# Kernel tuning notes

Measured on AMD Instinct MI355X. Metric: run time of the kernel, lower is better.

## Reference

```python
import jax, jax.numpy as jnp
import numpy as np

H = 1024       # hidden_size
R = 4          # downsacale_ratio -> bottleneck H//R = 256
DI = 2048      # mamba d_inner = expand * H
NS = 16        # d_state
KC = 4         # d_conv
DTR = 64       # dt_rank = ceil(H/16)
B, L = 4, 1024


def setup_inputs() -> dict:
    key = jax.random.key(0)
    ks = iter(jax.random.split(key, 32))
    w = lambda shape, s=0.02: jax.random.normal(next(ks), shape, jnp.float32) * s
    Hr = H // R
    inp = {
        'x': jax.random.normal(next(ks), (B, L, H), jnp.float32),
        't': jax.random.normal(next(ks), (B, H), jnp.float32),
        # adaLN modulation: SiLU -> Linear(H, 3H)
        'ada_w': w((H, 3 * H)), 'ada_b': jnp.zeros((3 * H,), jnp.float32),
        # hg_dense: Linear(H,H/R) SiLU Linear(H/R,H)
        'hgd_w1': w((H, Hr)), 'hgd_b1': jnp.zeros((Hr,), jnp.float32),
        'hgd_w2': w((Hr, H)), 'hgd_b2': jnp.zeros((H,), jnp.float32),
        # Mamba params
        'in_proj_w': w((H, 2 * DI)),
        'conv_w': w((DI, KC), 0.1), 'conv_b': jnp.zeros((DI,), jnp.float32),
        'x_proj_w': w((DI, DTR + 2 * NS)),
        'dt_proj_w': w((DTR, DI), 0.1),
        'dt_proj_b': jnp.log(jnp.expm1(jnp.full((DI,), 0.01, jnp.float32))),  # softplus^-1(0.01)
        'A_log': jnp.log(jnp.broadcast_to(jnp.arange(1, NS + 1, dtype=jnp.float32), (DI, NS))),
        'Dp': jnp.ones((DI,), jnp.float32),
        'out_proj_w': w((DI, H)),
        # hg_fuse
        'fm_w': w((H, Hr)), 'fm_b': jnp.zeros((Hr,), jnp.float32),
        'fr_w': w((H, Hr)), 'fr_b': jnp.zeros((Hr,), jnp.float32),
        'ff_w': w((Hr, H)), 'ff_b': jnp.zeros((H,), jnp.float32),
    }
    return inp


def _ln(x, eps=1e-6):
    mu = jnp.mean(x, -1, keepdims=True)
    var = jnp.mean(jnp.square(x - mu), -1, keepdims=True)
    return (x - mu) / jnp.sqrt(var + eps)


def _mamba(xd, in_proj_w, conv_w, conv_b, x_proj_w, dt_proj_w, dt_proj_b, A_log, Dp, out_proj_w):
    # xd: [B, L, H]
    xz = xd @ in_proj_w                      # [B, L, 2*DI]
    xm, z = jnp.split(xz, 2, axis=-1)
    # causal depthwise conv over time
    xc = jnp.swapaxes(xm, 1, 2)              # [B, DI, L]
    xc = jax.lax.conv_general_dilated(
        xc, conv_w[:, None, :], window_strides=(1,), padding=[(KC - 1, 0)],
        feature_group_count=DI, dimension_numbers=('NCH', 'OIH', 'NCH'))
    xc = jax.nn.silu(jnp.swapaxes(xc, 1, 2) + conv_b)   # [B, L, DI]
    dbl = xc @ x_proj_w                      # [B, L, DTR + 2*NS]
    dt = jax.nn.softplus(dbl[..., :DTR] @ dt_proj_w + dt_proj_b)   # [B, L, DI]
    Bm = dbl[..., DTR:DTR + NS]              # [B, L, NS]
    Cm = dbl[..., DTR + NS:]                 # [B, L, NS]
    A = -jnp.exp(A_log)                      # [DI, NS]

    def step(h, inp):
        dt_t, x_t, B_t, C_t = inp            # [B,DI],[B,DI],[B,NS],[B,NS]
        dA = jnp.exp(dt_t[:, :, None] * A)                       # [B, DI, NS]
        h = dA * h + (dt_t * x_t)[:, :, None] * B_t[:, None, :]
        y = jnp.einsum('bdn,bn->bd', h, C_t)
        return h, y

    h0 = jnp.zeros((xd.shape[0], DI, NS), xd.dtype)
    seq = (jnp.moveaxis(dt, 1, 0), jnp.moveaxis(xc, 1, 0),
           jnp.moveaxis(Bm, 1, 0), jnp.moveaxis(Cm, 1, 0))
    _, ys = jax.lax.scan(step, h0, seq)
    y = jnp.moveaxis(ys, 0, 1) + xc * Dp     # [B, L, DI]
    y = y * jax.nn.silu(z)
    return y @ out_proj_w                    # [B, L, H]


def reference(x, t, ada_w, ada_b, hgd_w1, hgd_b1, hgd_w2, hgd_b2,
              in_proj_w, conv_w, conv_b, x_proj_w, dt_proj_w, dt_proj_b,
              A_log, Dp, out_proj_w, fm_w, fm_b, fr_w, fr_b, ff_w, ff_b):
    ada = jax.nn.silu(t) @ ada_w + ada_b               # [B, 3H]
    shift, scale, alpha = jnp.split(ada, 3, axis=-1)
    x1 = _ln(x) * (1 + scale[:, None, :]) + shift[:, None, :]
    xd = jax.nn.silu(x1 @ hgd_w1 + hgd_b1) @ hgd_w2 + hgd_b2
    x1_2 = _mamba(xd, in_proj_w, conv_w, conv_b, x_proj_w, dt_proj_w,
                  dt_proj_b, A_log, Dp, out_proj_w)
    a = jax.nn.silu(x1_2 @ fm_w + fm_b)
    b = jax.nn.silu(x1 @ fr_w + fr_b)
    fuse = (a * b) @ ff_w + ff_b
    return x + alpha[:, None, :] * fuse
```

## Files before the change

kernel.cpp:

```cpp
#include <hip/hip_runtime.h>
#include <math.h>
#include <stdint.h>

#define H_   1024
#define HR_  256
#define DI_  2048
#define NS_  16
#define KC_  4
#define DTR_ 64
#define B_   4
#define L_   1024
#define ROWS (B_*L_)
#define H3_  3072
#define NCH_ 32
#define CL_  32
#define CLT_ 8

typedef short bf16x8 __attribute__((ext_vector_type(8)));
typedef float f32x4  __attribute__((ext_vector_type(4)));

#if __has_builtin(__builtin_amdgcn_exp2f)
#define EXP2(x) __builtin_amdgcn_exp2f(x)
#else
#define EXP2(x) __expf((x) * 0.6931471805599453f)
#endif
#define LOG2E 1.4426950408889634f

__device__ __forceinline__ float silu_f(float v) { return v / (1.f + __expf(-v)); }

__device__ __forceinline__ uint32_t pack_bf16_2(float a, float b) {
    uint32_t ua = __float_as_uint(a);
    uint32_t ub = __float_as_uint(b);
    uint32_t ra = (ua + 0x7FFFu + ((ua >> 16) & 1u)) >> 16;
    uint32_t rb = (ub + 0x7FFFu + ((ub >> 16) & 1u)) >> 16;
    return ra | (rb << 16);
}
__device__ __forceinline__ unsigned short cvt_bf16(float a) {
    uint32_t ua = __float_as_uint(a);
    return (unsigned short)((ua + 0x7FFFu + ((ua >> 16) & 1u)) >> 16);
}
__device__ __forceinline__ float bf16_to_f(unsigned short u) {
    return __uint_as_float(((uint32_t)u) << 16);
}

__device__ __forceinline__ void gload16(const short* g, short* l) {
    __builtin_amdgcn_global_load_lds(
        (const __attribute__((address_space(1))) void*)g,
        (__attribute__((address_space(3))) void*)l, 16, 0, 0);
}

#define TW_HGDFR 0ull
#define TW_HGD2  524288ull
#define TW_INPJ  786432ull
#define TW_XPJ   4980736ull
#define TW_DTPJ  5242880ull
#define TW_OPJ   5373952ull
#define TW_FM    7471104ull
#define TW_FF    7733248ull
#define TWT      7995392ull

__global__ __launch_bounds__(256) void wtrans_kernel(
    const float* __restrict__ s0, const float* __restrict__ s1,
    const float* __restrict__ s2, const float* __restrict__ s3,
    const float* __restrict__ s4, const float* __restrict__ s5,
    const float* __restrict__ s6, const float* __restrict__ s7,
    const float* __restrict__ s8, short* __restrict__ wt)
{
    int bid = blockIdx.x;
    const float* src; short* dst; int K, N, rel;
    if      (bid < 256)  { src = s0; dst = wt + TW_HGDFR;          K = 1024; N = 256;  rel = bid; }
    else if (bid < 512)  { src = s1; dst = wt + TW_HGDFR + 262144; K = 1024; N = 256;  rel = bid - 256; }
    else if (bid < 768)  { src = s2; dst = wt + TW_HGD2;           K = 256;  N = 1024; rel = bid - 512; }
    else if (bid < 4864) { src = s3; dst = wt + TW_INPJ;           K = 1024; N = 4096; rel = bid - 768; }
    else if (bid < 5120) { src = s4; dst = wt + TW_XPJ;            K = 2048; N = 96;   rel = bid - 4864; }
    else if (bid < 5248) { src = s5; dst = wt + TW_DTPJ;           K = 64;   N = 2048; rel = bid - 5120; }
    else if (bid < 7296) { src = s6; dst = wt + TW_OPJ;            K = 2048; N = 1024; rel = bid - 5248; }
    else if (bid < 7552) { src = s7; dst = wt + TW_FM;             K = 1024; N = 256;  rel = bid - 7296; }
    else                 { src = s8; dst = wt + TW_FF;             K = 256;  N = 1024; rel = bid - 7552; }
    int tkc = K >> 5;
    int tk = rel % tkc, tn = rel / tkc;

    __shared__ float ld[32][33];
    int tx = threadIdx.x & 7, ty = threadIdx.x >> 3;
    int kk = tk * 32 + ty, nn = tn * 32 + tx * 4;
    float4 v = make_float4(0.f, 0.f, 0.f, 0.f);
    if (nn < N) v = *(const float4*)&src[(size_t)kk * N + nn];
    ld[ty][tx * 4 + 0] = v.x; ld[ty][tx * 4 + 1] = v.y;
    ld[ty][tx * 4 + 2] = v.z; ld[ty][tx * 4 + 3] = v.w;
    __syncthreads();
    int nn2 = tn * 32 + ty, kk2 = tk * 32 + tx * 4;
    float a0 = ld[tx * 4 + 0][ty], a1 = ld[tx * 4 + 1][ty];
    float a2 = ld[tx * 4 + 2][ty], a3 = ld[tx * 4 + 3][ty];
    uint2 p = { pack_bf16_2(a0, a1), pack_bf16_2(a2, a3) };
    *(uint2*)&dst[(size_t)nn2 * K + kk2] = p;
}

__global__ __launch_bounds__(256) void cwt_kernel(
    const float* __restrict__ conv_w, float* __restrict__ cwt)
{
    int d = blockIdx.x * 256 + threadIdx.x;
    float4 v = *(const float4*)&conv_w[d * KC_];
    cwt[0 * DI_ + d] = v.x;
    cwt[1 * DI_ + d] = v.y;
    cwt[2 * DI_ + d] = v.z;
    cwt[3 * DI_ + d] = v.w;
}

__global__ __launch_bounds__(256) void ada_part_kernel(
    const float* __restrict__ t, const float* __restrict__ ada_w,
    float* __restrict__ part)
{
    int col = blockIdx.x * 1024 + threadIdx.x * 4;
    int b = blockIdx.y, z = blockIdx.z;
    __shared__ float st[32];
    if (threadIdx.x < 32) {
        float v = t[b * H_ + z * 32 + threadIdx.x];
        st[threadIdx.x] = silu_f(v);
    }
    __syncthreads();
    float4 acc = make_float4(0.f, 0.f, 0.f, 0.f);
    const float* w = ada_w + (size_t)(z * 32) * H3_ + col;
    #pragma unroll
    for (int k = 0; k < 32; ++k) {
        float4 wv = *(const float4*)(w + (size_t)k * H3_);
        float s = st[k];
        acc.x = fmaf(s, wv.x, acc.x);
        acc.y = fmaf(s, wv.y, acc.y);
        acc.z = fmaf(s, wv.z, acc.z);
        acc.w = fmaf(s, wv.w, acc.w);
    }
    *(float4*)&part[((size_t)z * B_ + b) * H3_ + col] = acc;
}

__global__ __launch_bounds__(256) void ada_red_kernel(
    const float* __restrict__ part, const float* __restrict__ ada_b,
    float* __restrict__ ada)
{
    int i = (blockIdx.x * 256 + threadIdx.x) * 4;
    int b = i / H3_, col = i - b * H3_;
    float4 s = make_float4(0.f, 0.f, 0.f, 0.f);
    #pragma unroll
    for (int z = 0; z < 32; ++z) {
        float4 p = *(const float4*)&part[((size_t)z * B_ + b) * H3_ + col];
        s.x += p.x; s.y += p.y; s.z += p.z; s.w += p.w;
    }
    float4 bv = *(const float4*)&ada_b[col];
    s.x += bv.x; s.y += bv.y; s.z += bv.z; s.w += bv.w;
    *(float4*)&ada[(size_t)b * H3_ + col] = s;
}

__global__ __launch_bounds__(256) void ln_mod_kernel(
    const float* __restrict__ x, const float* __restrict__ ada,
    short* __restrict__ x1b)
{
    int row = blockIdx.x;
    int b   = row >> 10;
    const float* xr = x + (size_t)row * H_;
    float4 v = ((const float4*)xr)[threadIdx.x];
    float s  = v.x + v.y + v.z + v.w;
    float s2 = v.x*v.x + v.y*v.y + v.z*v.z + v.w*v.w;

    __shared__ float red[8];
    int wave = threadIdx.x >> 6, lane = threadIdx.x & 63;
    #pragma unroll
    for (int off = 32; off; off >>= 1) {
        s  += __shfl_down(s,  off);
        s2 += __shfl_down(s2, off);
    }
    if (lane == 0) { red[wave] = s; red[4 + wave] = s2; }
    __syncthreads();
    float ts  = red[0] + red[1] + red[2] + red[3];
    float ts2 = red[4] + red[5] + red[6] + red[7];
    float mu  = ts  * (1.f / H_);
    float var = ts2 * (1.f / H_) - mu * mu;
    float inv = rsqrtf(var + 1e-6f);

    const float* sh = ada + b * H3_;
    int i = threadIdx.x * 4;
    float4 sh4 = *(const float4*)&sh[i];
    float4 sc4 = *(const float4*)&sh[H_ + i];
    float ox = (v.x - mu) * inv * (1.f + sc4.x) + sh4.x;
    float oy = (v.y - mu) * inv * (1.f + sc4.y) + sh4.y;
    float oz = (v.z - mu) * inv * (1.f + sc4.z) + sh4.z;
    float ow = (v.w - mu) * inv * (1.f + sc4.w) + sh4.w;
    uint2 p = { pack_bf16_2(ox, oy), pack_bf16_2(oz, ow) };
    *(uint2*)(x1b + (size_t)row * H_ + i) = p;
}

template<int ACT, bool SPLITK>
__global__ __launch_bounds__(256) void gemm128(
    const short* __restrict__ A, int lda,
    const short* __restrict__ Wt, int ldw,
    const float* __restrict__ bias,
    float* __restrict__ C, short* __restrict__ Cb, short* __restrict__ Cb2,
    int ldc, int M, int N, int K,
    const float* __restrict__ E0, const float* __restrict__ E1)
{
    __shared__ short As[3][4096];
    __shared__ short Bs[3][4096];
    int tid  = threadIdx.x;
    int lane = tid & 63, wv = tid >> 6, wm = wv >> 1, wn = wv & 1;
    int n0 = blockIdx.x * 128;
    int m0 = blockIdx.y * 128;

    if (SPLITK) {
        int z = blockIdx.z;
        A  += (size_t)z * K;
        Wt += (size_t)z * K;
        C  += (size_t)z * M * N;
    }

    int r = lane & 15, g = lane >> 4;
    int sA = wv * 2;
    const short* ga0 = A  + (size_t)(m0 + sA * 16 + r) * lda + g * 8;
    const short* ga1 = ga0 + (size_t)16 * lda;
    const short* gb0 = Wt + (size_t)(n0 + sA * 16 + r) * ldw + g * 8;
    const short* gb1 = gb0 + (size_t)16 * ldw;

    f32x4 acc[4][4];
    #pragma unroll
    for (int i = 0; i < 4; ++i)
        #pragma unroll
        for (int j = 0; j < 4; ++j) {
            acc[i][j][0] = 0.f; acc[i][j][1] = 0.f;
            acc[i][j][2] = 0.f; acc[i][j][3] = 0.f;
        }

    #define STAGE(buf, koff)                                    \
        do {                                                    \
            gload16(ga0 + (koff), &As[buf][sA * 512]);          \
            gload16(ga1 + (koff), &As[buf][sA * 512 + 512]);    \
            gload16(gb0 + (koff), &Bs[buf][sA * 512]);          \
            gload16(gb1 + (koff), &Bs[buf][sA * 512 + 512]);    \
        } while (0)

    #define COMPUTE(buf)                                                          \
        do {                                                                      \
            bf16x8 af[4], bfr[4];                                                 \
            _Pragma("unroll")                                                     \
            for (int i = 0; i < 4; ++i)                                           \
                af[i] = *(const bf16x8*)&As[buf][(wm * 4 + i) * 512 + lane * 8];  \
            _Pragma("unroll")                                                     \
            for (int j = 0; j < 4; ++j)                                           \
                bfr[j] = *(const bf16x8*)&Bs[buf][(wn * 4 + j) * 512 + lane * 8]; \
            _Pragma("unroll")                                                     \
            for (int i = 0; i < 4; ++i)                                           \
                _Pragma("unroll")                                                 \
                for (int j = 0; j < 4; ++j)                                       \
                    acc[i][j] = __builtin_amdgcn_mfma_f32_16x16x32_bf16(          \
                        af[i], bfr[j], acc[i][j], 0, 0, 0);                       \
        } while (0)

    int T = K >> 5;
    STAGE(0, 0);
    if (T > 1) STAGE(1, 32);
    for (int t = 0; t < T; ++t) {
        if (t + 1 < T) asm volatile("s_waitcnt vmcnt(4)" ::: "memory");
        else           asm volatile("s_waitcnt vmcnt(0)" ::: "memory");
        __builtin_amdgcn_s_barrier();
        if (t + 2 < T) STAGE((t + 2) % 3, (t + 2) * 32);
        COMPUTE(t % 3);
    }
    #undef STAGE
    #undef COMPUTE

    #pragma unroll
    for (int i = 0; i < 4; ++i) {
        int mb = m0 + wm * 64 + i * 16 + ((lane >> 4) << 2);
        #pragma unroll
        for (int j = 0; j < 4; ++j) {
            int n = n0 + wn * 64 + j * 16 + (lane & 15);
            if (n < N) {
                float bv;
                if (ACT == 6) bv = (n < 256) ? bias[n] : E0[n - 256];
                else          bv = bias ? bias[n] : 0.f;
                #pragma unroll
                for (int rr = 0; rr < 4; ++rr) {
                    int m = mb + rr;
                    float v = acc[i][j][rr] + bv;
                    size_t ci = (size_t)m * ldc + n;
                    if (ACT == 6) {
                        float sv = silu_f(v);
                        if (n < 256) Cb[(size_t)m * 256 + n]        = (short)cvt_bf16(sv);
                        else         Cb2[(size_t)m * 256 + (n-256)] = (short)cvt_bf16(sv);
                    } else {
                        if (ACT == 2) v = (v > 20.f) ? v : log1pf(__expf(v));
                        else if (ACT == 4) {
                            int bb = m >> 10;
                            v = E0[ci] + E1[bb * H3_ + 2 * H_ + n] * v;
                        }
                        if (C)  C[ci]  = v;
                        if (Cb) Cb[ci] = (short)cvt_bf16(v);
                    }
                }
            }
        }
    }
}

template<int ACT, bool SPLITK>
__global__ __launch_bounds__(512) void gemm256d(
    const short* __restrict__ A, int lda,
    const short* __restrict__ Wt, int ldw,
    short* __restrict__ Cb, int ldc,
    int M, int N, int K)
{
    extern __shared__ short lds[];
    short* Asb = lds;
    short* Bsb = lds + 16384;
    int tid  = threadIdx.x;
    int lane = tid & 63, wv = tid >> 6;
    int wm = wv >> 2, wn = wv & 3;
    int n0 = blockIdx.x * 256;
    int m0 = blockIdx.y * 256;

    if (SPLITK) {
        int z = blockIdx.z;
        A  += (size_t)z * K;
        Wt += (size_t)z * K;
        Cb += (size_t)z * M * N;
    }

    int r = lane & 15, g = lane >> 4;
    int sA = wv * 2;
    const short* ga0 = A  + (size_t)(m0 + sA * 16 + r) * lda + g * 8;
    const short* ga1 = ga0 + (size_t)16 * lda;
    const short* gb0 = Wt + (size_t)(n0 + sA * 16 + r) * ldw + g * 8;
    const short* gb1 = gb0 + (size_t)16 * ldw;

    f32x4 acc[8][4];
    #pragma unroll
    for (int i = 0; i < 8; ++i)
        #pragma unroll
        for (int j = 0; j < 4; ++j) {
            acc[i][j][0] = 0.f; acc[i][j][1] = 0.f;
            acc[i][j][2] = 0.f; acc[i][j][3] = 0.f;
        }

    #define STAGE2(buf, koff)                                       \
        do {                                                        \
            gload16(ga0 + (koff), &Asb[(buf) * 8192 + sA * 512]);   \
            gload16(ga1 + (koff), &Asb[(buf) * 8192 + sA * 512 + 512]); \
            gload16(gb0 + (koff), &Bsb[(buf) * 8192 + sA * 512]);   \
            gload16(gb1 + (koff), &Bsb[(buf) * 8192 + sA * 512 + 512]); \
        } while (0)

    int T = K >> 5;
    STAGE2(0, 0);
    __syncthreads();
    int cur = 0;
    for (int t = 0; t < T; ++t) {
        if (t + 1 < T) STAGE2(cur ^ 1, (t + 1) * 32);
        {
            bf16x8 af[8], bfr[4];
            #pragma unroll
            for (int i = 0; i < 8; ++i)
                af[i] = *(const bf16x8*)&Asb[cur * 8192 + (wm * 8 + i) * 512 + lane * 8];
            #pragma unroll
            for (int j = 0; j < 4; ++j)
                bfr[j] = *(const bf16x8*)&Bsb[cur * 8192 + (wn * 4 + j) * 512 + lane * 8];
            __builtin_amdgcn_s_setprio(1);
            #pragma unroll
            for (int i = 0; i < 8; ++i)
                #pragma unroll
                for (int j = 0; j < 4; ++j)
                    acc[i][j] = __builtin_amdgcn_mfma_f32_16x16x32_bf16(
                        af[i], bfr[j], acc[i][j], 0, 0, 0);
            __builtin_amdgcn_s_setprio(0);
        }
        __syncthreads();
        cur ^= 1;
    }
    #undef STAGE2

    #pragma unroll
    for (int i = 0; i < 8; ++i) {
        int mb = m0 + wm * 128 + i * 16 + ((lane >> 4) << 2);
        #pragma unroll
        for (int j = 0; j < 4; ++j) {
            int n = n0 + wn * 64 + j * 16 + (lane & 15);
            #pragma unroll
            for (int rr = 0; rr < 4; ++rr) {
                int m = mb + rr;
                float v = acc[i][j][rr];
                if (ACT == 5) {
                    size_t idx = (n < DI_) ? ((size_t)m * DI_ + n)
                                           : ((size_t)ROWS * DI_ + (size_t)m * DI_ + (n - DI_));
                    Cb[idx] = (short)cvt_bf16(v);
                } else if (ACT == 8) {
                    Cb[(size_t)m * ldc + n] = (short)cvt_bf16(v);
                }
            }
        }
    }
}

__global__ __launch_bounds__(256) void redk_xproj(
    const float* __restrict__ part, float* __restrict__ dbl,
    short* __restrict__ dblb)
{
    size_t i = ((size_t)blockIdx.x * 256 + threadIdx.x) * 4;
    const size_t seg = (size_t)ROWS * 96;
    float4 s = *(const float4*)(part + i);
    #pragma unroll
    for (int z = 1; z < 8; ++z) {
        float4 p = *(const float4*)(part + z * seg + i);
        s.x += p.x; s.y += p.y; s.z += p.z; s.w += p.w;
    }
    *(float4*)(dbl + i) = s;
    uint2 p = { pack_bf16_2(s.x, s.y), pack_bf16_2(s.z, s.w) };
    *(uint2*)(dblb + i) = p;
}

__global__ __launch_bounds__(256) void redk_op4(
    const short* __restrict__ part, short* __restrict__ x12b)
{
    size_t i = ((size_t)blockIdx.x * 256 + threadIdx.x) * 8;
    const size_t seg = (size_t)ROWS * H_;
    float s[8];
    bf16x8 p0 = *(const bf16x8*)(part + i);
    #pragma unroll
    for (int e = 0; e < 8; ++e) s[e] = bf16_to_f((unsigned short)p0[e]);
    #pragma unroll
    for (int z = 1; z < 4; ++z) {
        bf16x8 pz = *(const bf16x8*)(part + z * seg + i);
        #pragma unroll
        for (int e = 0; e < 8; ++e) s[e] += bf16_to_f((unsigned short)pz[e]);
    }
    bf16x8 o;
    #pragma unroll
    for (int e = 0; e < 8; ++e) o[e] = (short)cvt_bf16(s[e]);
    *(bf16x8*)(x12b + i) = o;
}

__global__ __launch_bounds__(256) void redk_fm(
    const float* __restrict__ part, const float* __restrict__ fm_b,
    const short* __restrict__ frlin, short* __restrict__ abb)
{
    size_t i = ((size_t)blockIdx.x * 256 + threadIdx.x) * 4;
    const size_t seg = (size_t)ROWS * HR_;
    float4 s = *(const float4*)(part + i);
    #pragma unroll
    for (int z = 1; z < 4; ++z) {
        float4 p = *(const float4*)(part + z * seg + i);
        s.x += p.x; s.y += p.y; s.z += p.z; s.w += p.w;
    }
    int col = (int)(i & (HR_ - 1));
    float4 b = *(const float4*)(fm_b + col);
    const short* fr = frlin + i;
    float o0 = silu_f(s.x + b.x) * bf16_to_f((unsigned short)fr[0]);
    float o1 = silu_f(s.y + b.y) * bf16_to_f((unsigned short)fr[1]);
    float o2 = silu_f(s.z + b.z) * bf16_to_f((unsigned short)fr[2]);
    float o3 = silu_f(s.w + b.w) * bf16_to_f((unsigned short)fr[3]);
    uint2 p = { pack_bf16_2(o0, o1), pack_bf16_2(o2, o3) };
    *(uint2*)(abb + i) = p;
}

__global__ __launch_bounds__(256) void conv_kernel(
    const short* __restrict__ xmb, const float* __restrict__ cwt,
    const float* __restrict__ conv_b, short* __restrict__ xcb)
{
    int d0 = threadIdx.x * 8;
    int b  = blockIdx.y;
    int l0 = blockIdx.x * CLT_;

    float w[KC_][8];
    #pragma unroll
    for (int j = 0; j < KC_; ++j) {
        float4 a = *(const float4*)&cwt[j * DI_ + d0];
        float4 c = *(const float4*)&cwt[j * DI_ + d0 + 4];
        w[j][0] = a.x; w[j][1] = a.y; w[j][2] = a.z; w[j][3] = a.w;
        w[j][4] = c.x; w[j][5] = c.y; w[j][6] = c.z; w[j][7] = c.w;
    }
    float bia[8];
    {
        float4 b0 = *(const float4*)&conv_b[d0];
        float4 b1 = *(const float4*)&conv_b[d0 + 4];
        bia[0] = b0.x; bia[1] = b0.y; bia[2] = b0.z; bia[3] = b0.w;
        bia[4] = b1.x; bia[5] = b1.y; bia[6] = b1.z; bia[7] = b1.w;
    }

    const short* base = xmb + (size_t)b * L_ * DI_ + d0;
    short*       outb = xcb + (size_t)b * L_ * DI_ + d0;

    bf16x8 win[KC_];
    #pragma unroll
    for (int j = 0; j < KC_ - 1; ++j) {
        int ll = l0 - (KC_ - 1) + j;
        if (ll >= 0) win[j] = *(const bf16x8*)(base + (size_t)ll * DI_);
        else         win[j] = (bf16x8)0;
    }
    for (int l = l0; l < l0 + CLT_; ++l) {
        win[KC_ - 1] = *(const bf16x8*)(base + (size_t)l * DI_);
        bf16x8 o;
        #pragma unroll
        for (int e = 0; e < 8; ++e) {
            float acc = bia[e];
            #pragma unroll
            for (int j = 0; j < KC_; ++j)
                acc = fmaf(bf16_to_f((unsigned short)win[j][e]), w[j][e], acc);
            o[e] = (short)cvt_bf16(silu_f(acc));
        }
        *(bf16x8*)(outb + (size_t)l * DI_) = o;
        win[0] = win[1]; win[1] = win[2]; win[2] = win[3];
    }
}

__global__ __launch_bounds__(256) void scan_part1(
    const short* __restrict__ dtb, const short* __restrict__ xcb,
    const float* __restrict__ dbl, const float* __restrict__ A_log,
    float* __restrict__ hend, float* __restrict__ dtsum)
{
    int bx = blockIdx.x;
    int dg = bx & 15;
    int bc = bx >> 4;
    int c  = bc & (NCH_ - 1);
    int b  = bc >> 5;
    int tid  = threadIdx.x;
    int lane = tid & 63, wv = tid >> 6;
    int dl   = tid >> 1;
    int d    = dg * 128 + dl;
    int half = tid & 1;
    int n0   = half * 8;

    __shared__ float sB[CL_][NS_];
    __shared__ short dtS[2][16][128];
    __shared__ short xcS[2][16][128];

    size_t srcoff = (size_t)(b * L_ + c * CL_ + wv * 4 + (lane >> 4)) * DI_
                    + dg * 128 + (lane & 15) * 8;
    const short* gdt = dtb + srcoff;
    const short* gxc = xcb + srcoff;

    #define SSTG1(buf, q)                                             \
        do {                                                          \
            gload16(gdt + (size_t)(q) * 16 * DI_, &dtS[buf][wv*4][0]); \
            gload16(gxc + (size_t)(q) * 16 * DI_, &xcS[buf][wv*4][0]); \
        } while (0)

    SSTG1(0, 0);
    for (int idx = tid; idx < CL_ * NS_; idx += 256) {
        int l = idx >> 4, n = idx & 15;
        sB[l][n] = dbl[(size_t)(b * L_ + c * CL_ + l) * 96 + DTR_ + n];
    }
    float Aa2[8];
    #pragma unroll
    for (int n = 0; n < 8; ++n)
        Aa2[n] = -__expf(A_log[d * NS_ + n0 + n]) * LOG2E;

    float h[8];
    #pragma unroll
    for (int n = 0; n < 8; ++n) h[n] = 0.f;
    float sdt = 0.f;

    __syncthreads();
    int buf = 0;
    for (int q = 0; q < 2; ++q) {
        if (q < 1) SSTG1(buf ^ 1, q + 1);
        #pragma unroll
        for (int li = 0; li < 16; ++li) {
            int l = q * 16 + li;
            float dtv = bf16_to_f((unsigned short)dtS[buf][li][dl]);
            float xv  = bf16_to_f((unsigned short)xcS[buf][li][dl]);
            float du  = dtv * xv;
            sdt += dtv;
            #pragma unroll
            for (int n = 0; n < 8; ++n)
                h[n] = fmaf(EXP2(dtv * Aa2[n]), h[n], du * sB[l][n0 + n]);
        }
        __syncthreads();
        buf ^= 1;
    }
    #undef SSTG1

    #pragma unroll
    for (int n = 0; n < 8; ++n)
        hend[((size_t)((b * NCH_ + c) * NS_ + n0 + n)) * DI_ + d] = h[n];
    if (half == 0)
        dtsum[(size_t)(b * NCH_ + c) * DI_ + d] = sdt;
}

__global__ __launch_bounds__(256) void scan_mid(
    const float* __restrict__ hend, const float* __restrict__ dtsum,
    const float* __restrict__ A_log, float* __restrict__ hin)
{
    int idx = blockIdx.x * 256 + threadIdx.x;
    int d  = idx & (DI_ - 1);
    int bn = idx >> 11;
    int n  = bn & (NS_ - 1);
    int b  = bn >> 4;
    float Aa2 = -__expf(A_log[d * NS_ + n]) * LOG2E;
    float h = 0.f;
    #pragma unroll
    for (int c = 0; c < NCH_; ++c) {
        size_t o = ((size_t)((b * NCH_ + c) * NS_ + n)) * DI_ + d;
        hin[o] = h;
        float s = dtsum[(size_t)(b * NCH_ + c) * DI_ + d];
        h = fmaf(EXP2(Aa2 * s), h, hend[o]);
    }
}

__global__ __launch_bounds__(256) void scan_part2(
    const short* __restrict__ dtb, const short* __restrict__ xcb,
    const short* __restrict__ zb, const float* __restrict__ dbl,
    const float* __restrict__ A_log, const float* __restrict__ Dp,
    const float* __restrict__ hin, short* __restrict__ y2b)
{
    int bx = blockIdx.x;
    int dg = bx & 15;
    int bc = bx >> 4;
    int c  = bc & (NCH_ - 1);
    int b  = bc >> 5;
    int tid  = threadIdx.x;
    int lane = tid & 63, wv = tid >> 6;
    int dl   = tid >> 1;
    int d    = dg * 128 + dl;
    int half = tid & 1;
    int n0   = half * 8;

    __shared__ float sBC[CL_][2 * NS_];
    __shared__ short dtS[2][16][128];
    __shared__ short xcS[2][16][128];
    __shared__ short zS[2][16][128];

    size_t srcoff = (size_t)(b * L_ + c * CL_ + wv * 4 + (lane >> 4)) * DI_
                    + dg * 128 + (lane & 15) * 8;
    const short* gdt = dtb + srcoff;
    const short* gxc = xcb + srcoff;
    const short* gz  = zb  + srcoff;

    #define SSTG2(buf, q)                                             \
        do {                                                          \
            gload16(gdt + (size_t)(q) * 16 * DI_, &dtS[buf][wv*4][0]); \
            gload16(gxc + (size_t)(q) * 16 * DI_, &xcS[buf][wv*4][0]); \
            gload16(gz  + (size_t)(q) * 16 * DI_, &zS[buf][wv*4][0]);  \
        } while (0)

    SSTG2(0, 0);
    for (int idx = tid; idx < CL_ * 2 * NS_; idx += 256) {
        int l = idx >> 5, n = idx & 31;
        sBC[l][n] = dbl[(size_t)(b * L_ + c * CL_ + l) * 96 + DTR_ + n];
    }
    float Aa2[8];
    #pragma unroll
    for (int n = 0; n < 8; ++n)
        Aa2[n] = -__expf(A_log[d * NS_ + n0 + n]) * LOG2E;

    float h[8];
    #pragma unroll
    for (int n = 0; n < 8; ++n)
        h[n] = hin[((size_t)((b * NCH_ + c) * NS_ + n0 + n)) * DI_ + d];
    float Dpv = Dp[d];
    size_t obase = (size_t)(b * L_ + c * CL_) * DI_ + d;

    __syncthreads();
    int buf = 0;
    for (int q = 0; q < 2; ++q) {
        if (q < 1) SSTG2(buf ^ 1, q + 1);
        #pragma unroll
        for (int li = 0; li < 16; ++li) {
            int l = q * 16 + li;
            float dtv = bf16_to_f((unsigned short)dtS[buf][li][dl]);
            float xv  = bf16_to_f((unsigned short)xcS[buf][li][dl]);
            float zv  = bf16_to_f((unsigned short)zS[buf][li][dl]);
            float du  = dtv * xv;
            float y = 0.f;
            #pragma unroll
            for (int n = 0; n < 8; ++n) {
                float dA = EXP2(dtv * Aa2[n]);
                h[n] = fmaf(dA, h[n], du * sBC[l][n0 + n]);
                y = fmaf(h[n], sBC[l][NS_ + n0 + n], y);
            }
            y += __shfl_xor(y, 1);
            if (half == 0) {
                y = fmaf(xv, Dpv, y);
                y2b[obase + (size_t)l * DI_] = (short)cvt_bf16(y * silu_f(zv));
            }
        }
        __syncthreads();
        buf ^= 1;
    }
    #undef SSTG2
}

extern "C" void kernel_launch(void* const* d_in, const int* in_sizes, int n_in,
                              void* d_out, int out_size, void* d_ws, size_t ws_size,
                              hipStream_t stream)
{
    const float* x         = (const float*)d_in[0];
    const float* t         = (const float*)d_in[1];
    const float* ada_w     = (const float*)d_in[2];
    const float* ada_b     = (const float*)d_in[3];
    const float* hgd_w1    = (const float*)d_in[4];
    const float* hgd_b1    = (const float*)d_in[5];
    const float* hgd_w2    = (const float*)d_in[6];
    const float* hgd_b2    = (const float*)d_in[7];
    const float* in_proj_w = (const float*)d_in[8];
    const float* conv_w    = (const float*)d_in[9];
    const float* conv_b    = (const float*)d_in[10];
    const float* x_proj_w  = (const float*)d_in[11];
    const float* dt_proj_w = (const float*)d_in[12];
    const float* dt_proj_b = (const float*)d_in[13];
    const float* A_log     = (const float*)d_in[14];
    const float* Dp        = (const float*)d_in[15];
    const float* out_proj_w= (const float*)d_in[16];
    const float* fm_w      = (const float*)d_in[17];
    const float* fm_b      = (const float*)d_in[18];
    const float* fr_w      = (const float*)d_in[19];
    const float* fr_b      = (const float*)d_in[20];
    const float* ff_w      = (const float*)d_in[21];
    const float* ff_b      = (const float*)d_in[22];
    float* out = (float*)d_out;

    char* p = (char*)d_ws;
    auto alloc = [&](size_t bytes) { char* r = p; p += (bytes + 255) & ~255ull; return r; };

    short* wt      = (short*)alloc(TWT * 2);
    float* cwt     = (float*)alloc((size_t)KC_ * DI_ * 4);
    short* x1b     = (short*)alloc((size_t)ROWS * H_ * 2);
    short* h1b     = (short*)alloc((size_t)ROWS * HR_ * 2);
    short* frlin   = (short*)alloc((size_t)ROWS * HR_ * 2);
    short* xdb     = (short*)alloc((size_t)ROWS * H_ * 2);
    short* xmzb    = (short*)alloc((size_t)ROWS * DI_ * 4);
    short* xcb     = (short*)alloc((size_t)ROWS * DI_ * 2);
    short* y2b     = (short*)alloc((size_t)ROWS * DI_ * 2);
    short* dtb     = (short*)alloc((size_t)ROWS * DI_ * 2);
    float* scratch = (float*)alloc((size_t)4 * ROWS * H_ * 4);
    float* dbl     = (float*)alloc((size_t)ROWS * 96 * 4);
    short* dblb    = (short*)alloc((size_t)ROWS * 96 * 2);
    short* x12b    = (short*)alloc((size_t)ROWS * H_ * 2);
    short* abb     = (short*)alloc((size_t)ROWS * HR_ * 2);
    float* ada     = (float*)alloc((size_t)B_ * H3_ * 4);

    short* xmb   = xmzb;
    short* zb    = xmzb + (size_t)ROWS * DI_;
    float* dtsum = (float*)abb;
    float* adapart = scratch;
    float* xppart  = scratch;
    float* hend    = scratch;
    float* hin     = scratch + (size_t)B_ * NCH_ * NS_ * DI_;
    short* oppart  = (short*)scratch;
    float* fmpart  = scratch;

    dim3 blk(256), b512(512);

    wtrans_kernel<<<dim3(7808), blk, 0, stream>>>(
        hgd_w1, fr_w, hgd_w2, in_proj_w, x_proj_w, dt_proj_w, out_proj_w,
        fm_w, ff_w, wt);
    cwt_kernel<<<dim3(DI_ / 256), blk, 0, stream>>>(conv_w, cwt);
    ada_part_kernel<<<dim3(3, B_, 32), blk, 0, stream>>>(t, ada_w, adapart);
    ada_red_kernel<<<dim3(B_ * H3_ / 4 / 256), blk, 0, stream>>>(adapart, ada_b, ada);
    ln_mod_kernel<<<dim3(ROWS), blk, 0, stream>>>(x, ada, x1b);
    gemm128<6, false><<<dim3(4, 32), blk, 0, stream>>>(
        x1b, H_, wt + TW_HGDFR, H_, hgd_b1, nullptr, h1b, frlin,
        512, ROWS, 512, H_, fr_b, nullptr);
    gemm128<0, false><<<dim3(8, 32), blk, 0, stream>>>(
        h1b, HR_, wt + TW_HGD2, HR_, hgd_b2, nullptr, xdb, nullptr,
        H_, ROWS, H_, HR_, nullptr, nullptr);
    gemm256d<5, false><<<dim3(16, 16), b512, 65536, stream>>>(
        xdb, H_, wt + TW_INPJ, H_, xmb, 2 * DI_, ROWS, 2 * DI_, H_);
    conv_kernel<<<dim3(L_ / CLT_, B_), blk, 0, stream>>>(xmb, cwt, conv_b, xcb);
    gemm128<0, true><<<dim3(1, 32, 8), blk, 0, stream>>>(
        xcb, DI_, wt + TW_XPJ, DI_, nullptr, xppart, nullptr, nullptr,
        96, ROWS, 96, 256, nullptr, nullptr);
    redk_xproj<<<dim3(ROWS * 96 / 4 / 256), blk, 0, stream>>>(xppart, dbl, dblb);
    gemm128<2, false><<<dim3(16, 32), blk, 0, stream>>>(
        dblb, 96, wt + TW_DTPJ, DTR_, dt_proj_b, nullptr, dtb, nullptr,
        DI_, ROWS, DI_, DTR_, nullptr, nullptr);
    scan_part1<<<dim3(B_ * NCH_ * 16), blk, 0, stream>>>(
        dtb, xcb, dbl, A_log, hend, dtsum);
    scan_mid<<<dim3(B_ * DI_ * NS_ / 256), blk, 0, stream>>>(
        hend, dtsum, A_log, hin);
    scan_part2<<<dim3(B_ * NCH_ * 16), blk, 0, stream>>>(
        dtb, xcb, zb, dbl, A_log, Dp, hin, y2b);
    gemm256d<8, true><<<dim3(4, 16, 4), b512, 65536, stream>>>(
        y2b, DI_, wt + TW_OPJ, DI_, oppart, H_, ROWS, H_, 512);
    redk_op4<<<dim3(ROWS * H_ / 8 / 256), blk, 0, stream>>>(oppart, x12b);
    gemm128<0, true><<<dim3(2, 32, 4), blk, 0, stream>>>(
        x12b, H_, wt + TW_FM, H_, nullptr, fmpart, nullptr, nullptr,
        HR_, ROWS, HR_, 256, nullptr, nullptr);
    redk_fm<<<dim3(ROWS * HR_ / 4 / 256), blk, 0, stream>>>(fmpart, fm_b, frlin, abb);
    gemm128<4, false><<<dim3(8, 32), blk, 0, stream>>>(
        abb, HR_, wt + TW_FF, HR_, ff_b, out, nullptr, nullptr,
        H_, ROWS, H_, HR_, x, ada);
}
```

Baseline: 352.1 us.

## Triple-buffer in_proj GEMM and split-K the hg_dense/fuse-reduce GEMM

Adds a gemm256 kernel with a three-stage LDS ring (96KB shared) that issues loads two k-steps ahead and uses a single barrier per iteration, replacing the double-buffered gemm256d for in_proj. It also splits the first hg_dense/fr GEMM over K into two partials, raising the grid from 128 to 256 blocks, and adds a reduction kernel that applies bias and SiLU. The pipelining aims to hide global load latency. The larger LDS footprint may reduce occupancy, and the split-K adds a partial-sum round trip through fp32 scratch.

```diff
diff --git a/kernel.cpp b/kernel.cpp
--- a/kernel.cpp
+++ b/kernel.cpp
@@ -298,6 +298,94 @@
     }
 }
 
+template<int ACT>
+__global__ __launch_bounds__(512) void gemm256(
+    const short* __restrict__ A, int lda,
+    const short* __restrict__ Wt, int ldw,
+    short* __restrict__ Cb, int M, int N, int K)
+{
+    extern __shared__ short lds[];
+    short* Asb = lds;
+    short* Bsb = lds + 24576;
+    int tid  = threadIdx.x;
+    int lane = tid & 63, wv = tid >> 6;
+    int wm = wv >> 2, wn = wv & 3;
+    int n0 = blockIdx.x * 256;
+    int m0 = blockIdx.y * 256;
+
+    int r = lane & 15, g = lane >> 4;
+    int sA = wv * 2;
+    const short* ga0 = A  + (size_t)(m0 + sA * 16 + r) * lda + g * 8;
+    const short* ga1 = ga0 + (size_t)16 * lda;
+    const short* gb0 = Wt + (size_t)(n0 + sA * 16 + r) * ldw + g * 8;
+    const short* gb1 = gb0 + (size_t)16 * ldw;
+
+    f32x4 acc[8][4];
+    #pragma unroll
+    for (int i = 0; i < 8; ++i)
+        #pragma unroll
+        for (int j = 0; j < 4; ++j) {
+            acc[i][j][0] = 0.f; acc[i][j][1] = 0.f;
+            acc[i][j][2] = 0.f; acc[i][j][3] = 0.f;
+        }
+
+    #define STAGE2(buf, koff)                                       \
+        do {                                                        \
+            gload16(ga0 + (koff), &Asb[(buf) * 8192 + sA * 512]);   \
+            gload16(ga1 + (koff), &Asb[(buf) * 8192 + sA * 512 + 512]); \
+            gload16(gb0 + (koff), &Bsb[(buf) * 8192 + sA * 512]);   \
+            gload16(gb1 + (koff), &Bsb[(buf) * 8192 + sA * 512 + 512]); \
+        } while (0)
+
+    int T = K >> 5;
+    STAGE2(0, 0);
+    if (T > 1) STAGE2(1, 32);
+    for (int t = 0; t < T; ++t) {
+        if (t + 1 < T) asm volatile("s_waitcnt vmcnt(4)" ::: "memory");
+        else           asm volatile("s_waitcnt vmcnt(0)" ::: "memory");
+        __builtin_amdgcn_s_barrier();
+        if (t + 2 < T) STAGE2((t + 2) % 3, (t + 2) * 32);
+        {
+            int buf = t % 3;
+            bf16x8 af[8], bfr[4];
+            #pragma unroll
+            for (int i = 0; i < 8; ++i)
+                af[i] = *(const bf16x8*)&Asb[buf * 8192 + (wm * 8 + i) * 512 + lane * 8];
+            #pragma unroll
+            for (int j = 0; j < 4; ++j)
+                bfr[j] = *(const bf16x8*)&Bsb[buf * 8192 + (wn * 4 + j) * 512 + lane * 8];
+            __builtin_amdgcn_s_setprio(1);
+            #pragma unroll
+            for (int i = 0; i < 8; ++i)
+                #pragma unroll
+                for (int j = 0; j < 4; ++j)
+                    acc[i][j] = __builtin_amdgcn_mfma_f32_16x16x32_bf16(
+                        af[i], bfr[j], acc[i][j], 0, 0, 0);
+            __builtin_amdgcn_s_setprio(0);
+        }
+    }
+    #undef STAGE2
+
+    #pragma unroll
+    for (int i = 0; i < 8; ++i) {
+        int mb = m0 + wm * 128 + i * 16 + ((lane >> 4) << 2);
+        #pragma unroll
+        for (int j = 0; j < 4; ++j) {
+            int n = n0 + wn * 64 + j * 16 + (lane & 15);
+            #pragma unroll
+            for (int rr = 0; rr < 4; ++rr) {
+                int m = mb + rr;
+                float v = acc[i][j][rr];
+                if (ACT == 5) {
+                    size_t idx = (n < DI_) ? ((size_t)m * DI_ + n)
+                                           : ((size_t)ROWS * DI_ + (size_t)m * DI_ + (n - DI_));
+                    Cb[idx] = (short)cvt_bf16(v);
+                }
+            }
+        }
+    }
+}
+
 template<int ACT, bool SPLITK>
 __global__ __launch_bounds__(512) void gemm256d(
     const short* __restrict__ A, int lda,
@@ -383,11 +471,7 @@
             for (int rr = 0; rr < 4; ++rr) {
                 int m = mb + rr;
                 float v = acc[i][j][rr];
-                if (ACT == 5) {
-                    size_t idx = (n < DI_) ? ((size_t)m * DI_ + n)
-                                           : ((size_t)ROWS * DI_ + (size_t)m * DI_ + (n - DI_));
-                    Cb[idx] = (short)cvt_bf16(v);
-                } else if (ACT == 8) {
+                if (ACT == 8) {
                     Cb[(size_t)m * ldc + n] = (short)cvt_bf16(v);
                 }
             }
@@ -410,6 +494,28 @@
     *(float4*)(dbl + i) = s;
     uint2 p = { pack_bf16_2(s.x, s.y), pack_bf16_2(s.z, s.w) };
     *(uint2*)(dblb + i) = p;
+}
+
+__global__ __launch_bounds__(256) void redk_hgdfr(
+    const float* __restrict__ part, const float* __restrict__ hgd_b1,
+    const float* __restrict__ fr_b, short* __restrict__ h1b,
+    short* __restrict__ frlin)
+{
+    size_t i = ((size_t)blockIdx.x * 256 + threadIdx.x) * 4;
+    const size_t seg = (size_t)ROWS * 512;
+    int m   = (int)(i >> 9);
+    int col = (int)(i & 511);
+    float4 a = *(const float4*)(part + i);
+    float4 b = *(const float4*)(part + seg + i);
+    float s0 = a.x + b.x, s1 = a.y + b.y, s2 = a.z + b.z, s3 = a.w + b.w;
+    const float* bias = (col < 256) ? (hgd_b1 + col) : (fr_b + col - 256);
+    float4 bv = *(const float4*)bias;
+    float o0 = silu_f(s0 + bv.x), o1 = silu_f(s1 + bv.y);
+    float o2 = silu_f(s2 + bv.z), o3 = silu_f(s3 + bv.w);
+    uint2 p = { pack_bf16_2(o0, o1), pack_bf16_2(o2, o3) };
+    short* dst = (col < 256) ? (h1b + (size_t)m * 256 + col)
+                             : (frlin + (size_t)m * 256 + col - 256);
+    *(uint2*)dst = p;
 }
 
 __global__ __launch_bounds__(256) void redk_op4(
@@ -736,6 +842,7 @@
     short* zb    = xmzb + (size_t)ROWS * DI_;
     float* dtsum = (float*)abb;
     float* adapart = scratch;
+    float* hfpart  = scratch;
     float* xppart  = scratch;
     float* hend    = scratch;
     float* hin     = scratch + (size_t)B_ * NCH_ * NS_ * DI_;
@@ -751,14 +858,16 @@
     ada_part_kernel<<<dim3(3, B_, 32), blk, 0, stream>>>(t, ada_w, adapart);
     ada_red_kernel<<<dim3(B_ * H3_ / 4 / 256), blk, 0, stream>>>(adapart, ada_b, ada);
     ln_mod_kernel<<<dim3(ROWS), blk, 0, stream>>>(x, ada, x1b);
-    gemm128<6, false><<<dim3(4, 32), blk, 0, stream>>>(
-        x1b, H_, wt + TW_HGDFR, H_, hgd_b1, nullptr, h1b, frlin,
-        512, ROWS, 512, H_, fr_b, nullptr);
+    gemm128<0, true><<<dim3(4, 32, 2), blk, 0, stream>>>(
+        x1b, H_, wt + TW_HGDFR, H_, nullptr, hfpart, nullptr, nullptr,
+        512, ROWS, 512, 512, nullptr, nullptr);
+    redk_hgdfr<<<dim3(ROWS * 512 / 4 / 256), blk, 0, stream>>>(
+        hfpart, hgd_b1, fr_b, h1b, frlin);
     gemm128<0, false><<<dim3(8, 32), blk, 0, stream>>>(
         h1b, HR_, wt + TW_HGD2, HR_, hgd_b2, nullptr, xdb, nullptr,
         H_, ROWS, H_, HR_, nullptr, nullptr);
-    gemm256d<5, false><<<dim3(16, 16), b512, 65536, stream>>>(
-        xdb, H_, wt + TW_INPJ, H_, xmb, 2 * DI_, ROWS, 2 * DI_, H_);
+    gemm256<5><<<dim3(16, 16), b512, 98304, stream>>>(
+        xdb, H_, wt + TW_INPJ, H_, xmb, ROWS, 2 * DI_, H_);
     conv_kernel<<<dim3(L_ / CLT_, B_), blk, 0, stream>>>(xmb, cwt, conv_b, xcb);
     gemm128<0, true><<<dim3(1, 32, 8), blk, 0, stream>>>(
         xcb, DI_, wt + TW_XPJ, DI_, nullptr, xppart, nullptr, nullptr,
```

Result: faster. 334.1 us (-5.1%).

## Triple-buffer gemm256 LDS pipeline and split-K the hgd/fr projection

Applied to the files above, without the earlier changes.

The 256x256 GEMM moves from double to triple buffering in LDS (96KB). Loads are now issued two K-steps ahead, and a single barrier per iteration is gated on explicit vmcnt waits, which removes one __syncthreads per step and deepens latency hiding. Separately, the first x1 projection (hgd_w1 and fr_w) is split-K over 2 slices with a new reduction kernel that applies bias and SiLU, giving that small grid more parallelism. The costs are more LDS per block, which may lower occupancy, an extra kernel launch, and a round trip of fp32 partials through memory.

```diff
diff --git a/kernel.cpp b/kernel.cpp
--- a/kernel.cpp
+++ b/kernel.cpp
@@ -299,15 +299,14 @@
 }
 
 template<int ACT, bool SPLITK>
-__global__ __launch_bounds__(512) void gemm256d(
+__global__ __launch_bounds__(512) void gemm256(
     const short* __restrict__ A, int lda,
     const short* __restrict__ Wt, int ldw,
-    short* __restrict__ Cb, int ldc,
-    int M, int N, int K)
+    short* __restrict__ Cb, int ldc, int M, int N, int K)
 {
     extern __shared__ short lds[];
     short* Asb = lds;
-    short* Bsb = lds + 16384;
+    short* Bsb = lds + 24576;
     int tid  = threadIdx.x;
     int lane = tid & 63, wv = tid >> 6;
     int wm = wv >> 2, wn = wv & 3;
@@ -347,18 +346,21 @@
 
     int T = K >> 5;
     STAGE2(0, 0);
-    __syncthreads();
-    int cur = 0;
+    if (T > 1) STAGE2(1, 32);
     for (int t = 0; t < T; ++t) {
-        if (t + 1 < T) STAGE2(cur ^ 1, (t + 1) * 32);
+        if (t + 1 < T) asm volatile("s_waitcnt vmcnt(4)" ::: "memory");
+        else           asm volatile("s_waitcnt vmcnt(0)" ::: "memory");
+        __builtin_amdgcn_s_barrier();
+        if (t + 2 < T) STAGE2((t + 2) % 3, (t + 2) * 32);
         {
+            int buf = t % 3;
             bf16x8 af[8], bfr[4];
             #pragma unroll
             for (int i = 0; i < 8; ++i)
-                af[i] = *(const bf16x8*)&Asb[cur * 8192 + (wm * 8 + i) * 512 + lane * 8];
+                af[i] = *(const bf16x8*)&Asb[buf * 8192 + (wm * 8 + i) * 512 + lane * 8];
             #pragma unroll
             for (int j = 0; j < 4; ++j)
-                bfr[j] = *(const bf16x8*)&Bsb[cur * 8192 + (wn * 4 + j) * 512 + lane * 8];
+                bfr[j] = *(const bf16x8*)&Bsb[buf * 8192 + (wn * 4 + j) * 512 + lane * 8];
             __builtin_amdgcn_s_setprio(1);
             #pragma unroll
             for (int i = 0; i < 8; ++i)
@@ -368,8 +370,6 @@
                         af[i], bfr[j], acc[i][j], 0, 0, 0);
             __builtin_amdgcn_s_setprio(0);
         }
-        __syncthreads();
-        cur ^= 1;
     }
     #undef STAGE2
 
@@ -410,6 +410,28 @@
     *(float4*)(dbl + i) = s;
     uint2 p = { pack_bf16_2(s.x, s.y), pack_bf16_2(s.z, s.w) };
     *(uint2*)(dblb + i) = p;
+}
+
+__global__ __launch_bounds__(256) void redk_hgdfr(
+    const float* __restrict__ part, const float* __restrict__ hgd_b1,
+    const float* __restrict__ fr_b, short* __restrict__ h1b,
+    short* __restrict__ frlin)
+{
+    size_t i = ((size_t)blockIdx.x * 256 + threadIdx.x) * 4;
+    const size_t seg = (size_t)ROWS * 512;
+    int m   = (int)(i >> 9);
+    int col = (int)(i & 511);
+    float4 a = *(const float4*)(part + i);
+    float4 b = *(const float4*)(part + seg + i);
+    float s0 = a.x + b.x, s1 = a.y + b.y, s2 = a.z + b.z, s3 = a.w + b.w;
+    const float* bias = (col < 256) ? (hgd_b1 + col) : (fr_b + col - 256);
+    float4 bv = *(const float4*)bias;
+    float o0 = silu_f(s0 + bv.x), o1 = silu_f(s1 + bv.y);
+    float o2 = silu_f(s2 + bv.z), o3 = silu_f(s3 + bv.w);
+    uint2 p = { pack_bf16_2(o0, o1), pack_bf16_2(o2, o3) };
+    short* dst = (col < 256) ? (h1b + (size_t)m * 256 + col)
+                             : (frlin + (size_t)m * 256 + col - 256);
+    *(uint2*)dst = p;
 }
 
 __global__ __launch_bounds__(256) void redk_op4(
@@ -736,6 +758,7 @@
     short* zb    = xmzb + (size_t)ROWS * DI_;
     float* dtsum = (float*)abb;
     float* adapart = scratch;
+    float* hfpart  = scratch;
     float* xppart  = scratch;
     float* hend    = scratch;
     float* hin     = scratch + (size_t)B_ * NCH_ * NS_ * DI_;
@@ -751,14 +774,16 @@
     ada_part_kernel<<<dim3(3, B_, 32), blk, 0, stream>>>(t, ada_w, adapart);
     ada_red_kernel<<<dim3(B_ * H3_ / 4 / 256), blk, 0, stream>>>(adapart, ada_b, ada);
     ln_mod_kernel<<<dim3(ROWS), blk, 0, stream>>>(x, ada, x1b);
-    gemm128<6, false><<<dim3(4, 32), blk, 0, stream>>>(
-        x1b, H_, wt + TW_HGDFR, H_, hgd_b1, nullptr, h1b, frlin,
-        512, ROWS, 512, H_, fr_b, nullptr);
+    gemm128<0, true><<<dim3(4, 32, 2), blk, 0, stream>>>(
+        x1b, H_, wt + TW_HGDFR, H_, nullptr, hfpart, nullptr, nullptr,
+        512, ROWS, 512, 512, nullptr, nullptr);
+    redk_hgdfr<<<dim3(ROWS * 512 / 4 / 256), blk, 0, stream>>>(
+        hfpart, hgd_b1, fr_b, h1b, frlin);
     gemm128<0, false><<<dim3(8, 32), blk, 0, stream>>>(
         h1b, HR_, wt + TW_HGD2, HR_, hgd_b2, nullptr, xdb, nullptr,
         H_, ROWS, H_, HR_, nullptr, nullptr);
-    gemm256d<5, false><<<dim3(16, 16), b512, 65536, stream>>>(
-        xdb, H_, wt + TW_INPJ, H_, xmb, 2 * DI_, ROWS, 2 * DI_, H_);
+    gemm256<5, false><<<dim3(16, 16), b512, 98304, stream>>>(
+        xdb, H_, wt + TW_INPJ, H_, xmb, 0, ROWS, 2 * DI_, H_);
     conv_kernel<<<dim3(L_ / CLT_, B_), blk, 0, stream>>>(xmb, cwt, conv_b, xcb);
     gemm128<0, true><<<dim3(1, 32, 8), blk, 0, stream>>>(
         xcb, DI_, wt + TW_XPJ, DI_, nullptr, xppart, nullptr, nullptr,
@@ -773,7 +798,7 @@
         hend, dtsum, A_log, hin);
     scan_part2<<<dim3(B_ * NCH_ * 16), blk, 0, stream>>>(
         dtb, xcb, zb, dbl, A_log, Dp, hin, y2b);
-    gemm256d<8, true><<<dim3(4, 16, 4), b512, 65536, stream>>>(
+    gemm256<8, true><<<dim3(4, 16, 4), b512, 98304, stream>>>(
         y2b, DI_, wt + TW_OPJ, DI_, oppart, H_, ROWS, H_, 512);
     redk_op4<<<dim3(ROWS * H_ / 8 / 256), blk, 0, stream>>>(oppart, x12b);
     gemm128<0, true><<<dim3(2, 32, 4), blk, 0, stream>>>(
```

After: 327.9 us, median of 2. -6.9%, faster.
